# Kernel tuning notes

Measured on AMD Instinct MI355X. Metric: run time of the kernel, lower is better.

Reference implementation:

```python
import jax, jax.numpy as jnp
import numpy as np


def _chamfer_one(x, y):
    # x: [N,3], y: [M,3]; squared-Euclidean pairwise distances via norm expansion
    x2 = jnp.sum(x * x, axis=-1)  # [N]
    y2 = jnp.sum(y * y, axis=-1)  # [M]
    cross = jnp.einsum('nd,md->nm', x, y)  # [N,M]
    d = x2[:, None] + y2[None, :] - 2.0 * cross  # [N,M] squared distances
    # kaolin chamfer_distance: mean of NN sq-dists in both directions, summed (w1=w2=1)
    return jnp.mean(jnp.min(d, axis=1)) + jnp.mean(jnp.min(d, axis=0))


def reference(x, y):
    # x, y: [B, N, 3] / [B, M, 3]
    per_sample = jax.vmap(_chamfer_one)(x, y)  # [B]
    return jnp.mean(per_sample)


def setup_inputs() -> dict:
    key = jax.random.key(0)
    kx, ky = jax.random.split(key)
    x = jax.random.normal(kx, (16, 4096, 3), dtype=jnp.float32)
    y = jax.random.normal(ky, (16, 4096, 3), dtype=jnp.float32)
    return {"x": x, "y": y}
```

## Files before the change

### kernel.cpp

```cpp
#include <hip/hip_runtime.h>
#include <hip/hip_fp16.h>
#include <math.h>


typedef _Float16 f16x8  __attribute__((ext_vector_type(8)));
typedef float    f32x16 __attribute__((ext_vector_type(16)));

constexpr int BATCH  = 16;
constexpr int NPTS   = 4096;
constexpr int NDB    = 2 * BATCH;
constexpr int CHUNK  = 1024;
constexpr int NCHUNK = NPTS / CHUNK;
constexpr int NBLK   = NDB * 32;

__device__ __forceinline__ void cvt_point(float a, float b, float c,
                                          _Float16& ha, _Float16& hb,
                                          _Float16& hc, _Float16& shi,
                                          _Float16& slo) {
    ha = (_Float16)a; hb = (_Float16)b; hc = (_Float16)c;
    float fa = (float)ha, fb = (float)hb, fc = (float)hc;
    float ss = fa * fa + fb * fb + fc * fc;
    shi = (_Float16)ss;
    slo = (_Float16)(ss - (float)shi);
}

__global__ void __launch_bounds__(256, 4)
chamfer_fused(const float* __restrict__ x, const float* __restrict__ y,
              float* __restrict__ partial) {
    const int bid  = blockIdx.x;
    const int qgrp = bid & 31;
    const int db   = bid >> 5;
    const int dir  = db >> 4;
    const int batch = db & (BATCH - 1);
    const int lane = threadIdx.x & 63;
    const int wave = threadIdx.x >> 6;
    const int m    = lane & 31;

    const float* P  = dir ? y : x;
    const float* G  = dir ? x : y;
    const float* Pb = P + (size_t)batch * NPTS * 3;
    const float* Gb = G + (size_t)batch * NPTS * 3;

    const _Float16 one = (_Float16)1.0f, zz = (_Float16)0.0f;
    f16x8 bfrag;
    {
        int qi = (qgrp * 4 + wave) * 32 + m;
        _Float16 ha, hb, hc, shi, slo;
        cvt_point(Pb[3 * qi], Pb[3 * qi + 1], Pb[3 * qi + 2],
                  ha, hb, hc, shi, slo);
        bfrag = (f16x8){ ha, hb, hc, one, one, shi, slo, zz };
    }

    __shared__ f16x8 As[CHUNK];

    const f32x16 z = {0.0f, 0.0f, 0.0f, 0.0f, 0.0f, 0.0f, 0.0f, 0.0f,
                      0.0f, 0.0f, 0.0f, 0.0f, 0.0f, 0.0f, 0.0f, 0.0f};
    float acc0 = INFINITY, acc1 = INFINITY;

    for (int ch = 0; ch < NCHUNK; ++ch) {
        __syncthreads();
        #pragma unroll
        for (int r = 0; r < CHUNK / 256; ++r) {
            int s = r * 256 + threadIdx.x;
            int j = ch * CHUNK + s;
            _Float16 ha, hb, hc, shi, slo;
            cvt_point(Gb[3 * j], Gb[3 * j + 1], Gb[3 * j + 2],
                      ha, hb, hc, shi, slo);
            As[s] = (f16x8){ (_Float16)(-2.0f * (float)ha),
                             (_Float16)(-2.0f * (float)hb),
                             (_Float16)(-2.0f * (float)hc),
                             shi, slo, one, one, zz };
        }
        __syncthreads();

        #pragma unroll 4
        for (int tt = 0; tt < CHUNK / 32; ++tt) {
            f16x8 af = As[tt * 32 + m];
            f32x16 d = __builtin_amdgcn_mfma_f32_32x32x16_f16(af, bfrag, z,
                                                              0, 0, 0);
            acc0 = fminf(fminf(d[0],  d[1]),  acc0);
            acc1 = fminf(fminf(d[8],  d[9]),  acc1);
            acc0 = fminf(fminf(d[2],  d[3]),  acc0);
            acc1 = fminf(fminf(d[10], d[11]), acc1);
            acc0 = fminf(fminf(d[4],  d[5]),  acc0);
            acc1 = fminf(fminf(d[12], d[13]), acc1);
            acc0 = fminf(fminf(d[6],  d[7]),  acc0);
            acc1 = fminf(fminf(d[14], d[15]), acc1);
        }
    }
    float acc = fminf(acc0, acc1);

    acc = fminf(acc, __shfl_xor(acc, 32, 64));
    #pragma unroll
    for (int off = 1; off < 64; off <<= 1) acc += __shfl_xor(acc, off, 64);

    __shared__ float s4[4];
    if (lane == 0) s4[wave] = acc;
    __syncthreads();
    if (threadIdx.x == 0)
        partial[bid] = (s4[0] + s4[1]) + (s4[2] + s4[3]);
}

__global__ void __launch_bounds__(256)
finalize(const float* __restrict__ partial, float* __restrict__ out) {
    float s = partial[threadIdx.x] + partial[threadIdx.x + 256] +
              partial[threadIdx.x + 512] + partial[threadIdx.x + 768];
    #pragma unroll
    for (int off = 32; off > 0; off >>= 1) s += __shfl_down(s, off, 64);
    __shared__ float ws_s[4];
    if ((threadIdx.x & 63) == 0) ws_s[threadIdx.x >> 6] = s;
    __syncthreads();
    if (threadIdx.x == 0) {
        float b = (ws_s[0] + ws_s[1]) + (ws_s[2] + ws_s[3]);
        out[0] = b * (0.25f / ((float)BATCH * (float)NPTS));
    }
}

extern "C" void kernel_launch(void* const* d_in, const int* in_sizes, int n_in,
                              void* d_out, int out_size, void* d_ws, size_t ws_size,
                              hipStream_t stream) {
    const float* x = (const float*)d_in[0];
    const float* y = (const float*)d_in[1];
    float* out = (float*)d_out;
    float* partial = (float*)d_ws;

    hipLaunchKernelGGL(chamfer_fused, dim3(NBLK), dim3(256), 0, stream,
                       x, y, partial);
    hipLaunchKernelGGL(finalize, dim3(1), dim3(256), 0, stream, partial, out);
}
```

Before: 75.02 us.

## Double-buffer target chunks in LDS and double queries per block

Target points are now staged into two LDS buffers. The next chunk is converted and written while the current one feeds the MFMA loop, which removes one barrier per chunk and hides the global-load latency behind compute. Blocks grow to 512 threads covering 256 queries, so each target chunk is loaded and converted half as often across the grid. The grid is halved, the chunk size is halved, and finalize now sums 512 partials. Occupancy per CU stays roughly the same, but there are fewer blocks to balance across CUs.

Result: faster. 73.42 us (-2.1%).

```diff
diff --git a/kernel.cpp b/kernel.cpp
--- a/kernel.cpp
+++ b/kernel.cpp
@@ -9,9 +9,11 @@
 constexpr int BATCH  = 16;
 constexpr int NPTS   = 4096;
 constexpr int NDB    = 2 * BATCH;
-constexpr int CHUNK  = 1024;
+constexpr int BLOCK  = 512;
+constexpr int QPB    = 256;
+constexpr int CHUNK  = 512;
 constexpr int NCHUNK = NPTS / CHUNK;
-constexpr int NBLK   = NDB * 32;
+constexpr int NBLK   = NDB * (NPTS / QPB);
 
 __device__ __forceinline__ void cvt_point(float a, float b, float c,
                                           _Float16& ha, _Float16& hb,
@@ -24,17 +26,17 @@
     slo = (_Float16)(ss - (float)shi);
 }
 
-__global__ void __launch_bounds__(256, 4)
+__global__ void __launch_bounds__(BLOCK, 4)
 chamfer_fused(const float* __restrict__ x, const float* __restrict__ y,
               float* __restrict__ partial) {
-    const int bid  = blockIdx.x;
-    const int qgrp = bid & 31;
-    const int db   = bid >> 5;
-    const int dir  = db >> 4;
+    const int bid   = blockIdx.x;
+    const int qgrp  = bid & 15;
+    const int db    = bid >> 4;
+    const int dir   = db >> 4;
     const int batch = db & (BATCH - 1);
-    const int lane = threadIdx.x & 63;
-    const int wave = threadIdx.x >> 6;
-    const int m    = lane & 31;
+    const int lane  = threadIdx.x & 63;
+    const int wave  = threadIdx.x >> 6;
+    const int m     = lane & 31;
 
     const float* P  = dir ? y : x;
     const float* G  = dir ? x : y;
@@ -42,16 +44,28 @@
     const float* Gb = G + (size_t)batch * NPTS * 3;
 
     const _Float16 one = (_Float16)1.0f, zz = (_Float16)0.0f;
+
     f16x8 bfrag;
     {
-        int qi = (qgrp * 4 + wave) * 32 + m;
+        int qi = qgrp * QPB + wave * 32 + m;
         _Float16 ha, hb, hc, shi, slo;
         cvt_point(Pb[3 * qi], Pb[3 * qi + 1], Pb[3 * qi + 2],
                   ha, hb, hc, shi, slo);
         bfrag = (f16x8){ ha, hb, hc, one, one, shi, slo, zz };
     }
 
-    __shared__ f16x8 As[CHUNK];
+    __shared__ f16x8 As[2][CHUNK];
+
+    {
+        int j = threadIdx.x;
+        _Float16 ha, hb, hc, shi, slo;
+        cvt_point(Gb[3 * j], Gb[3 * j + 1], Gb[3 * j + 2],
+                  ha, hb, hc, shi, slo);
+        As[0][threadIdx.x] = (f16x8){ (_Float16)(-2.0f * (float)ha),
+                                      (_Float16)(-2.0f * (float)hb),
+                                      (_Float16)(-2.0f * (float)hc),
+                                      shi, slo, one, one, zz };
+    }
 
     const f32x16 z = {0.0f, 0.0f, 0.0f, 0.0f, 0.0f, 0.0f, 0.0f, 0.0f,
                       0.0f, 0.0f, 0.0f, 0.0f, 0.0f, 0.0f, 0.0f, 0.0f};
@@ -59,23 +73,20 @@
 
     for (int ch = 0; ch < NCHUNK; ++ch) {
         __syncthreads();
-        #pragma unroll
-        for (int r = 0; r < CHUNK / 256; ++r) {
-            int s = r * 256 + threadIdx.x;
-            int j = ch * CHUNK + s;
+        const int cur = ch & 1;
+        if (ch + 1 < NCHUNK) {
+            int j = (ch + 1) * CHUNK + threadIdx.x;
             _Float16 ha, hb, hc, shi, slo;
             cvt_point(Gb[3 * j], Gb[3 * j + 1], Gb[3 * j + 2],
                       ha, hb, hc, shi, slo);
-            As[s] = (f16x8){ (_Float16)(-2.0f * (float)ha),
-                             (_Float16)(-2.0f * (float)hb),
-                             (_Float16)(-2.0f * (float)hc),
-                             shi, slo, one, one, zz };
+            As[cur ^ 1][threadIdx.x] = (f16x8){ (_Float16)(-2.0f * (float)ha),
+                                                (_Float16)(-2.0f * (float)hb),
+                                                (_Float16)(-2.0f * (float)hc),
+                                                shi, slo, one, one, zz };
         }
-        __syncthreads();
-
         #pragma unroll 4
         for (int tt = 0; tt < CHUNK / 32; ++tt) {
-            f16x8 af = As[tt * 32 + m];
+            f16x8 af = As[cur][tt * 32 + m];
             f32x16 d = __builtin_amdgcn_mfma_f32_32x32x16_f16(af, bfrag, z,
                                                               0, 0, 0);
             acc0 = fminf(fminf(d[0],  d[1]),  acc0);
@@ -94,17 +105,19 @@
     #pragma unroll
     for (int off = 1; off < 64; off <<= 1) acc += __shfl_xor(acc, off, 64);
 
-    __shared__ float s4[4];
-    if (lane == 0) s4[wave] = acc;
+    __shared__ float s8[8];
+    if (lane == 0) s8[wave] = acc;
     __syncthreads();
-    if (threadIdx.x == 0)
-        partial[bid] = (s4[0] + s4[1]) + (s4[2] + s4[3]);
+    if (threadIdx.x == 0) {
+        float b = ((s8[0] + s8[1]) + (s8[2] + s8[3])) +
+                  ((s8[4] + s8[5]) + (s8[6] + s8[7]));
+        partial[bid] = b;
+    }
 }
 
 __global__ void __launch_bounds__(256)
 finalize(const float* __restrict__ partial, float* __restrict__ out) {
-    float s = partial[threadIdx.x] + partial[threadIdx.x + 256] +
-              partial[threadIdx.x + 512] + partial[threadIdx.x + 768];
+    float s = partial[threadIdx.x] + partial[threadIdx.x + 256];
     #pragma unroll
     for (int off = 32; off > 0; off >>= 1) s += __shfl_down(s, off, 64);
     __shared__ float ws_s[4];
@@ -124,7 +137,7 @@
     float* out = (float*)d_out;
     float* partial = (float*)d_ws;
 
-    hipLaunchKernelGGL(chamfer_fused, dim3(NBLK), dim3(256), 0, stream,
+    hipLaunchKernelGGL(chamfer_fused, dim3(NBLK), dim3(BLOCK), 0, stream,
                        x, y, partial);
     hipLaunchKernelGGL(finalize, dim3(1), dim3(256), 0, stream, partial, out);
 }
```
